# Kernel optimization log

Hardware: AMD Instinct MI355X
Metric: run time of the kernel (lower is better)

The kernel has to match this reference:

```python
import jax, jax.numpy as jnp
import numpy as np
import math

B, T, C, H = 2, 2048, 1024, 16
D = C // H

def setup_inputs() -> dict:
    key = jax.random.key(0)
    ks = jax.random.split(key, 10)
    s = 1.0 / math.sqrt(C)
    return {
        "x": jax.random.normal(ks[0], (B, T, C), jnp.float32),
        "x_query": jax.random.normal(ks[1], (B, T, C), jnp.float32),
        "Wq": jax.random.normal(ks[2], (C, C), jnp.float32) * s,
        "bq": jax.random.normal(ks[3], (C,), jnp.float32) * 0.02,
        "Wk": jax.random.normal(ks[4], (C, C), jnp.float32) * s,
        "bk": jax.random.normal(ks[5], (C,), jnp.float32) * 0.02,
        "Wv": jax.random.normal(ks[6], (C, C), jnp.float32) * s,
        "bv": jax.random.normal(ks[7], (C,), jnp.float32) * 0.02,
        "Wp": jax.random.normal(ks[8], (C, C), jnp.float32) * s,
        "bp": jax.random.normal(ks[9], (C,), jnp.float32) * 0.02,
    }

def reference(x, x_query, Wq, bq, Wk, bk, Wv, bv, Wp, bp):
    # torch nn.Linear: y = x @ W^T + b
    Tq = x_query.shape[1]
    Tk = x.shape[1]
    q = (x_query @ Wq.T + bq).reshape(B, Tq, H, D).transpose(0, 2, 1, 3)  # [B,H,Tq,D]
    k = (x @ Wk.T + bk).reshape(B, Tk, H, D).transpose(0, 2, 1, 3)       # [B,H,Tk,D]
    v = (x @ Wv.T + bv).reshape(B, Tk, H, D).transpose(0, 2, 1, 3)       # [B,H,Tk,D]
    scale = 1.0 / math.sqrt(D)
    att = jnp.einsum('bhqd,bhkd->bhqk', q, k) * scale                    # [B,H,Tq,Tk]
    # use_mask=True, past_kv=None -> causal tril mask over (Tq, Tk)
    mask = jnp.tril(jnp.ones((Tq, Tk), dtype=bool))
    att = jnp.where(mask[None, None, :, :], att, -jnp.inf)
    att = jax.nn.softmax(att, axis=-1)
    y = jnp.einsum('bhqk,bhkd->bhqd', att, v)                            # [B,H,Tq,D]
    y = y.transpose(0, 2, 1, 3).reshape(B, Tq, C)
    y = y @ Wp.T + bp
    return y
```

## Files before the change

kernel.cpp:

```cpp
#include <hip/hip_runtime.h>

typedef __bf16 bf16;
typedef __attribute__((ext_vector_type(8))) __bf16 bf16x8;
typedef __attribute__((ext_vector_type(4))) float f32x4;
typedef __attribute__((ext_vector_type(16))) float f32x16;
typedef __attribute__((ext_vector_type(4))) unsigned u32x4;

#define MFMA16(a, b, c) __builtin_amdgcn_mfma_f32_16x16x32_bf16((a), (b), (c), 0, 0, 0)
#define MFMA32(a, b, c) __builtin_amdgcn_mfma_f32_32x32x16_bf16((a), (b), (c), 0, 0, 0)
#define NEG_BIG (-1e30f)
#define SCL_LOG2 0.18033688011112042f
#define THR_RAW 44.3614195558365f

__device__ __forceinline__ void gload_lds16(void* lds, const void* g) {
  __builtin_amdgcn_global_load_lds(
      (const __attribute__((address_space(1))) void*)g,
      (__attribute__((address_space(3))) void*)lds, 16, 0, 0);
}

__device__ __forceinline__ unsigned pk2(float x, float y) {
  const unsigned short a = __builtin_bit_cast(unsigned short, (bf16)x);
  const unsigned short b = __builtin_bit_cast(unsigned short, (bf16)y);
  return (unsigned)a | ((unsigned)b << 16);
}

static __device__ const signed char KQT[32] =
  {15,15,10,10, 15,14,14,14,13, 9, 9, 4, 13,13,12,12, 8, 8,
   12,11,11,11, 7, 7, 3,  6, 6,  5, 5, 2,  1,  0};
static __device__ const signed char KSEG[32] =
  { 0, 1, 0, 1,  2, 0, 1, 2, 0, 0, 1, 0,  1, 2, 0, 1, 0, 1,
    2, 0, 1, 2, 0, 1, 0,  0, 1,  0, 1, 0,  0,  0};

__global__ void cvt6(const float* __restrict__ s0, const float* __restrict__ s1,
                     const float* __restrict__ s2, const float* __restrict__ s3,
                     const float* __restrict__ s4, const float* __restrict__ s5,
                     bf16* __restrict__ d0, bf16* __restrict__ d1,
                     bf16* __restrict__ d2, bf16* __restrict__ d3,
                     bf16* __restrict__ d4, bf16* __restrict__ d5) {
  const int c = blockIdx.x * blockDim.x + threadIdx.x;
  if (c >= 1572864) return;
  const float* s; bf16* d; int off;
  if (c < 524288)        { s = s0; d = d0; off = c; }
  else if (c < 1048576)  { s = s1; d = d1; off = c - 524288; }
  else {
    const int c2 = c - 1048576, seg = c2 >> 17;
    off = c2 & 131071;
    s = seg == 0 ? s2 : seg == 1 ? s3 : seg == 2 ? s4 : s5;
    d = seg == 0 ? d2 : seg == 1 ? d3 : seg == 2 ? d4 : d5;
  }
  const float4 a = ((const float4*)s)[off * 2 + 0];
  const float4 b = ((const float4*)s)[off * 2 + 1];
  bf16x8 o;
  o[0] = (bf16)a.x; o[1] = (bf16)a.y; o[2] = (bf16)a.z; o[3] = (bf16)a.w;
  o[4] = (bf16)b.x; o[5] = (bf16)b.y; o[6] = (bf16)b.z; o[7] = (bf16)b.w;
  ((bf16x8*)d)[off] = o;
}

__global__ void gemm_qkv(const bf16* __restrict__ XQ, const bf16* __restrict__ X,
                         const bf16* __restrict__ Wq, const bf16* __restrict__ Wk,
                         const bf16* __restrict__ Wv,
                         const float* __restrict__ bq, const float* __restrict__ bk,
                         const float* __restrict__ bv,
                         bf16* __restrict__ Qo, bf16* __restrict__ Ko,
                         bf16* __restrict__ Vto) {
  __shared__ __align__(16) bf16 As[128 * 32];
  __shared__ __align__(16) bf16 Bs[128 * 32];
  const int tid = threadIdx.x;
  const int wv = tid >> 6, lane = tid & 63;
  const int wr = wv >> 1, wc = wv & 1;
  const int lr = lane & 15, lg = lane >> 4;
  const int seg = blockIdx.x >> 3;
  const int n0 = (blockIdx.x & 7) * 128;
  const int m0 = blockIdx.y * 128;
  const bf16* __restrict__ A = seg == 0 ? XQ : X;
  const bf16* __restrict__ W = seg == 0 ? Wq : seg == 1 ? Wk : Wv;
  const float* __restrict__ bias = seg == 0 ? bq : seg == 1 ? bk : bv;
  const int K = 1024;

  f32x4 acc[4][4] = {};

  for (int k0 = 0; k0 < K; k0 += 32) {
    __syncthreads();
#pragma unroll
    for (int j = 0; j < 2; ++j) {
      const int e8 = (j * 256 + tid) * 8;
      const int row = e8 >> 5, col = e8 & 31;
      gload_lds16(As + (size_t)(j * 256 + wv * 64) * 8,
                  A + (size_t)(m0 + row) * K + k0 + col);
      gload_lds16(Bs + (size_t)(j * 256 + wv * 64) * 8,
                  W + (size_t)(n0 + row) * K + k0 + col);
    }
    __syncthreads();
    bf16x8 af[4], bfr[4];
#pragma unroll
    for (int i = 0; i < 4; ++i)
      af[i] = *(const bf16x8*)&As[(wr * 64 + i * 16 + lr) * 32 + lg * 8];
#pragma unroll
    for (int j = 0; j < 4; ++j)
      bfr[j] = *(const bf16x8*)&Bs[(wc * 64 + j * 16 + lr) * 32 + lg * 8];
#pragma unroll
    for (int i = 0; i < 4; ++i)
#pragma unroll
      for (int j = 0; j < 4; ++j)
        acc[i][j] = MFMA16(af[i], bfr[j], acc[i][j]);
  }

#pragma unroll
  for (int j = 0; j < 4; ++j) {
    const int n = n0 + wc * 64 + j * 16 + lr;
    const float bvv = bias[n];
    const int h = n >> 6, d = n & 63;
#pragma unroll
    for (int i = 0; i < 4; ++i) {
#pragma unroll
      for (int r = 0; r < 4; ++r) {
        const int m = m0 + wr * 64 + i * 16 + lg * 4 + r;
        const float v = acc[i][j][r] + bvv;
        const int b = m >> 11, t = m & 2047;
        if (seg == 0)      Qo[((size_t)(b * 16 + h) * 2048 + t) * 64 + d] = (bf16)v;
        else if (seg == 1) Ko[((size_t)(b * 16 + h) * 2048 + t) * 64 + d] = (bf16)v;
        else               Vto[((size_t)(b * 16 + h) * 64 + d) * 2048 + t] = (bf16)v;
      }
    }
  }
}

template <int BN>
__global__ void gemm_out(const bf16* __restrict__ A, const bf16* __restrict__ W,
                         const float* __restrict__ bias, float* __restrict__ out,
                         int M, int N, int K) {
  __shared__ __align__(16) bf16 As[128 * 32];
  __shared__ __align__(16) bf16 Bs[BN * 32];
  constexpr int NF = BN / 32;
  const int tid = threadIdx.x;
  const int wv = tid >> 6, lane = tid & 63;
  const int wr = wv >> 1, wc = wv & 1;
  const int lr = lane & 15, lg = lane >> 4;
  const int m0 = blockIdx.y * 128, n0 = blockIdx.x * BN;

  f32x4 acc[4][NF] = {};

  for (int k0 = 0; k0 < K; k0 += 32) {
    __syncthreads();
#pragma unroll
    for (int j = 0; j < 2; ++j) {
      const int e8 = (j * 256 + tid) * 8;
      const int row = e8 >> 5, col = e8 & 31;
      gload_lds16(As + (size_t)(j * 256 + wv * 64) * 8,
                  A + (size_t)(m0 + row) * K + k0 + col);
    }
#pragma unroll
    for (int j = 0; j < BN / 64; ++j) {
      const int e8 = (j * 256 + tid) * 8;
      const int row = e8 >> 5, col = e8 & 31;
      gload_lds16(Bs + (size_t)(j * 256 + wv * 64) * 8,
                  W + (size_t)(n0 + row) * K + k0 + col);
    }
    __syncthreads();
    bf16x8 af[4], bfr[NF];
#pragma unroll
    for (int i = 0; i < 4; ++i)
      af[i] = *(const bf16x8*)&As[(wr * 64 + i * 16 + lr) * 32 + lg * 8];
#pragma unroll
    for (int j = 0; j < NF; ++j)
      bfr[j] = *(const bf16x8*)&Bs[(wc * (BN / 2) + j * 16 + lr) * 32 + lg * 8];
#pragma unroll
    for (int i = 0; i < 4; ++i)
#pragma unroll
      for (int j = 0; j < NF; ++j)
        acc[i][j] = MFMA16(af[i], bfr[j], acc[i][j]);
  }

#pragma unroll
  for (int j = 0; j < NF; ++j) {
    const int n = n0 + wc * (BN / 2) + j * 16 + lr;
    const float bv = bias[n];
#pragma unroll
    for (int i = 0; i < 4; ++i) {
#pragma unroll
      for (int r = 0; r < 4; ++r) {
        const int m = m0 + wr * 64 + i * 16 + lg * 4 + r;
        out[(size_t)m * N + n] = acc[i][j][r] + bv;
      }
    }
  }
}

__global__ void attn_fwd(const bf16* __restrict__ Q, const bf16* __restrict__ Kk,
                         const bf16* __restrict__ Vt, bf16* __restrict__ attout,
                         bf16* __restrict__ Opart, float* __restrict__ Ml) {
  __shared__ __align__(16) char Ks[2][8192];
  __shared__ __align__(16) char Vs[2][8192];

  const int tid = threadIdx.x;
  const int wv = tid >> 6, lane = tid & 63;
  const int q31 = lane & 31, hi = lane >> 5, l7 = lane & 7;
  const int kind = blockIdx.x >> 5, bh = blockIdx.x & 31;
  const int qt = KQT[kind], seg = KSEG[kind];
  const int nt = 2 * qt + 2;
  const int ns = qt >= 11 ? 3 : (qt >= 5 ? 2 : 1);
  const int t0 = (nt * seg) / ns, t1 = (nt * (seg + 1)) / ns;
  const bool split = ns > 1;

  const int q0 = qt * 128;
  const int qs = q0 + wv * 32;
  const int qa = qs + q31;
  const size_t bhT = (size_t)bh * 2048;
  const bf16* Vh = Vt + (size_t)bh * 64 * 2048;

  bf16x8 qf[4];
#pragma unroll
  for (int kw = 0; kw < 4; ++kw)
    qf[kw] = *(const bf16x8*)(Q + (bhT + qa) * 64 + kw * 16 + hi * 8);

  u32x4 onesu; onesu[0] = onesu[1] = onesu[2] = onesu[3] = 0x3F803F80u;
  const bf16x8 ones8 = __builtin_bit_cast(bf16x8, onesu);

  f32x16 O0 = {}, O1 = {};
  f32x16 Ol = {};
  float m2 = NEG_BIG;

  auto STAGE = [&](int buf, int kv0) {
#pragma unroll
    for (int rr = 0; rr < 2; ++rr) {
      const int c = rr * 256 + tid;
      const int row = c >> 3, cc = c & 7;
      const int gcol = (cc ^ (row & 7)) * 8;
      gload_lds16(Ks[buf] + (rr * 256 + wv * 64) * 16,
                  Kk + (bhT + kv0 + row) * 64 + gcol);
      gload_lds16(Vs[buf] + (rr * 256 + wv * 64) * 16,
                  Vh + (size_t)row * 2048 + kv0 + gcol);
    }
  };

  STAGE(0, t0 * 64);
  __syncthreads();

  for (int it = t0; it < t1; ++it) {
    const int kv0 = it * 64;
    const int cur = (it - t0) & 1;
    if (it + 1 < t1) STAGE(cur ^ 1, (it + 1) * 64);

    if (kv0 <= qs + 31) {
      f32x16 S0 = {}, S1 = {};
      __builtin_amdgcn_s_setprio(1);
#pragma unroll
      for (int kw = 0; kw < 4; ++kw) {
        const int cb = (32 * kw + 16 * hi) ^ (l7 << 4);
        const bf16x8 k0 = *(const bf16x8*)(Ks[cur] + q31 * 128 + cb);
        const bf16x8 k1 = *(const bf16x8*)(Ks[cur] + (32 + q31) * 128 + cb);
        S0 = MFMA32(k0, qf[kw], S0);
        S1 = MFMA32(k1, qf[kw], S1);
      }
      __builtin_amdgcn_s_setprio(0);

      float p[32];
#pragma unroll
      for (int r = 0; r < 16; ++r) { p[r] = S0[r]; p[16 + r] = S1[r]; }
      if (kv0 + 63 > qs) {
#pragma unroll
        for (int a = 0; a < 2; ++a)
#pragma unroll
          for (int r = 0; r < 16; ++r) {
            const int kva = kv0 + a * 32 + (r & 3) + 8 * (r >> 2) + 4 * hi;
            if (kva > qa) p[a * 16 + r] = NEG_BIG;
          }
      }

      float w16[16];
#pragma unroll
      for (int i = 0; i < 16; ++i) w16[i] = fmaxf(p[i], p[i + 16]);
#pragma unroll
      for (int i = 0; i < 8; ++i) w16[i] = fmaxf(w16[i], w16[i + 8]);
#pragma unroll
      for (int i = 0; i < 4; ++i) w16[i] = fmaxf(w16[i], w16[i + 4]);
      float mx = fmaxf(fmaxf(w16[0], w16[1]), fmaxf(w16[2], w16[3]));
      mx = fmaxf(mx, __shfl_xor(mx, 32));
      if (!__all(mx - m2 <= THR_RAW)) {
        const float mnew = fmaxf(m2, mx);
        const float fac = exp2f((m2 - mnew) * SCL_LOG2);
#pragma unroll
        for (int r = 0; r < 16; ++r) { O0[r] *= fac; O1[r] *= fac; }
        Ol[0] *= fac;
        m2 = mnew;
      }
      const float nm2 = -m2 * SCL_LOG2;
#pragma unroll
      for (int i = 0; i < 32; ++i) p[i] = exp2f(__builtin_fmaf(p[i], SCL_LOG2, nm2));

      bf16x8 pf[4];
#pragma unroll
      for (int ks = 0; ks < 4; ++ks) {
        const int base = 16 * (ks >> 1) + 8 * (ks & 1);
        const unsigned g0 = pk2(p[base + 0], p[base + 1]);
        const unsigned g1 = pk2(p[base + 2], p[base + 3]);
        const unsigned g2 = pk2(p[base + 4], p[base + 5]);
        const unsigned g3 = pk2(p[base + 6], p[base + 7]);
        const unsigned e0 = __shfl_xor(hi ? g0 : g2, 32);
        const unsigned e1 = __shfl_xor(hi ? g1 : g3, 32);
        u32x4 w4;
        w4[0] = hi ? e0 : g0;
        w4[1] = hi ? e1 : g1;
        w4[2] = hi ? g2 : e0;
        w4[3] = hi ? g3 : e1;
        pf[ks] = __builtin_bit_cast(bf16x8, w4);
      }

      __builtin_amdgcn_s_setprio(1);
#pragma unroll
      for (int ks = 0; ks < 4; ++ks) {
        const int cb = (32 * ks + 16 * hi) ^ (l7 << 4);
        const bf16x8 v0 = *(const bf16x8*)(Vs[cur] + q31 * 128 + cb);
        const bf16x8 v1 = *(const bf16x8*)(Vs[cur] + (32 + q31) * 128 + cb);
        O0 = MFMA32(v0, pf[ks], O0);
        O1 = MFMA32(v1, pf[ks], O1);
        Ol = MFMA32(ones8, pf[ks], Ol);
      }
      __builtin_amdgcn_s_setprio(0);
    }
    __syncthreads();
  }

  const float l = Ol[0];
  if (!split) {
    const int b = bh >> 4, h = bh & 15;
    const float inv = 1.f / l;
    bf16* orow = attout + ((size_t)b * 2048 + qa) * 1024 + h * 64;
#pragma unroll
    for (int r = 0; r < 16; ++r) {
      const int dd = (r & 3) + 8 * (r >> 2) + 4 * hi;
      orow[dd]      = (bf16)(O0[r] * inv);
      orow[32 + dd] = (bf16)(O1[r] * inv);
    }
  } else {
    const int sbase = (qt < 11) ? (qt - 5) * 2 : 12 + (qt - 11) * 3;
    const int slot = bh * 27 + sbase + seg;
    bf16* Po = Opart + (size_t)slot * 8192;
    const int row = wv * 32 + q31;
#pragma unroll
    for (int r = 0; r < 16; ++r) {
      const int dd = (r & 3) + 8 * (r >> 2) + 4 * hi;
      Po[row * 64 + dd]      = (bf16)O0[r];
      Po[row * 64 + 32 + dd] = (bf16)O1[r];
    }
    Ml[slot * 256 + row]       = m2;
    Ml[slot * 256 + 128 + row] = l;
  }
}

__global__ void attn_combine(const bf16* __restrict__ Opart,
                             const float* __restrict__ Ml,
                             bf16* __restrict__ attout) {
  const int u = blockIdx.x;
  const int bh = u / 11, qti = u - bh * 11;
  const int qt = qti + 5;
  const int ns = qt >= 11 ? 3 : 2;
  const int sbase = (qt < 11) ? (qt - 5) * 2 : 12 + (qt - 11) * 3;
  const int s0 = bh * 27 + sbase;
  const int tid = threadIdx.x;
  const int row = tid >> 1, c0 = (tid & 1) * 32;

  float m[3], lv[3];
  float M = NEG_BIG;
#pragma unroll
  for (int s = 0; s < 3; ++s)
    if (s < ns) {
      m[s] = Ml[(s0 + s) * 256 + row];
      lv[s] = Ml[(s0 + s) * 256 + 128 + row];
      M = fmaxf(M, m[s]);
    }
  float w[3], L = 0.f;
#pragma unroll
  for (int s = 0; s < 3; ++s)
    if (s < ns) {
      w[s] = exp2f((m[s] - M) * SCL_LOG2);
      L += w[s] * lv[s];
    }
  const float inv = 1.f / L;

  float acc[32] = {};
#pragma unroll
  for (int s = 0; s < 3; ++s)
    if (s < ns) {
      const bf16* p = Opart + (size_t)(s0 + s) * 8192 + row * 64 + c0;
      const float ws = w[s];
#pragma unroll
      for (int j = 0; j < 4; ++j) {
        const bf16x8 v = *(const bf16x8*)(p + j * 8);
#pragma unroll
        for (int e = 0; e < 8; ++e) acc[j * 8 + e] += ws * (float)v[e];
      }
    }

  const int b = bh >> 4, h = bh & 15, t = qt * 128 + row;
  bf16* dst = attout + ((size_t)b * 2048 + t) * 1024 + h * 64 + c0;
#pragma unroll
  for (int d = 0; d < 32; ++d) dst[d] = (bf16)(acc[d] * inv);
}

extern "C" void kernel_launch(void* const* d_in, const int* in_sizes, int n_in,
                              void* d_out, int out_size, void* d_ws, size_t ws_size,
                              hipStream_t stream) {
  const float* x   = (const float*)d_in[0];
  const float* xq  = (const float*)d_in[1];
  const float* Wq  = (const float*)d_in[2];
  const float* bq  = (const float*)d_in[3];
  const float* Wk  = (const float*)d_in[4];
  const float* bk  = (const float*)d_in[5];
  const float* Wv  = (const float*)d_in[6];
  const float* bv  = (const float*)d_in[7];
  const float* Wp  = (const float*)d_in[8];
  const float* bp  = (const float*)d_in[9];
  float* out = (float*)d_out;

  const size_t NTC = 4194304;
  const size_t NW  = 1048576;
  bf16* ws = (bf16*)d_ws;
  bf16* XQb = ws;
  bf16* Xb  = XQb + NTC;
  bf16* Wqb = Xb + NTC;
  bf16* Wkb = Wqb + NW;
  bf16* Wvb = Wkb + NW;
  bf16* Wpb = Wvb + NW;
  bf16* Qw  = Wpb + NW;
  bf16* Kw  = Qw + NTC;
  bf16* Vtw = Kw + NTC;
  bf16* Aw  = Vtw + NTC;
  bf16* Opart = (bf16*)d_ws;
  float* Ml   = (float*)(Aw + NTC);

  dim3 blk(256);
  cvt6<<<dim3(6144), blk, 0, stream>>>(xq, x, Wq, Wk, Wv, Wp,
                                       XQb, Xb, Wqb, Wkb, Wvb, Wpb);
  gemm_qkv<<<dim3(24, 32), blk, 0, stream>>>(XQb, Xb, Wqb, Wkb, Wvb,
                                             bq, bk, bv, Qw, Kw, Vtw);
  attn_fwd<<<dim3(1024), blk, 0, stream>>>(Qw, Kw, Vtw, Aw, Opart, Ml);
  attn_combine<<<dim3(352), blk, 0, stream>>>(Opart, Ml, Aw);
  gemm_out<64><<<dim3(16, 32), blk, 0, stream>>>(Aw, Wpb, bp, out, 4096, 1024, 1024);
}
```

Before: 128.2 us.

## Double GEMM K-tile to 64 with XOR-swizzled LDS layout

Both projection GEMMs now stage a 64-wide K slice per iteration instead of 32, halving the number of barrier pairs and global-load issue rounds. The LDS rows are 128 bytes, so the 16-byte chunks are XOR-swizzled by row to avoid bank conflicts on the MFMA fragment reads. Each staged tile is consumed in two MFMA halves. Shared memory per block grows (32KB for qkv), which may lower occupancy, and the gemm_out template parameter is removed in favor of a fixed BN of 64.

```diff
diff --git a/kernel.cpp b/kernel.cpp
--- a/kernel.cpp
+++ b/kernel.cpp
@@ -63,8 +63,8 @@
                          const float* __restrict__ bv,
                          bf16* __restrict__ Qo, bf16* __restrict__ Ko,
                          bf16* __restrict__ Vto) {
-  __shared__ __align__(16) bf16 As[128 * 32];
-  __shared__ __align__(16) bf16 Bs[128 * 32];
+  __shared__ __align__(16) char As[128 * 128];
+  __shared__ __align__(16) char Bs[128 * 128];
   const int tid = threadIdx.x;
   const int wv = tid >> 6, lane = tid & 63;
   const int wr = wv >> 1, wc = wv & 1;
@@ -79,30 +79,39 @@
 
   f32x4 acc[4][4] = {};
 
-  for (int k0 = 0; k0 < K; k0 += 32) {
+  for (int k0 = 0; k0 < K; k0 += 64) {
     __syncthreads();
 #pragma unroll
-    for (int j = 0; j < 2; ++j) {
-      const int e8 = (j * 256 + tid) * 8;
-      const int row = e8 >> 5, col = e8 & 31;
-      gload_lds16(As + (size_t)(j * 256 + wv * 64) * 8,
-                  A + (size_t)(m0 + row) * K + k0 + col);
-      gload_lds16(Bs + (size_t)(j * 256 + wv * 64) * 8,
-                  W + (size_t)(n0 + row) * K + k0 + col);
+    for (int j = 0; j < 4; ++j) {
+      const int c = j * 256 + tid;
+      const int row = c >> 3, cc = c & 7;
+      const int gcol = (cc ^ (row & 7)) * 8;
+      gload_lds16(As + (j * 256 + wv * 64) * 16,
+                  A + (size_t)(m0 + row) * K + k0 + gcol);
+      gload_lds16(Bs + (j * 256 + wv * 64) * 16,
+                  W + (size_t)(n0 + row) * K + k0 + gcol);
     }
     __syncthreads();
-    bf16x8 af[4], bfr[4];
-#pragma unroll
-    for (int i = 0; i < 4; ++i)
-      af[i] = *(const bf16x8*)&As[(wr * 64 + i * 16 + lr) * 32 + lg * 8];
-#pragma unroll
-    for (int j = 0; j < 4; ++j)
-      bfr[j] = *(const bf16x8*)&Bs[(wc * 64 + j * 16 + lr) * 32 + lg * 8];
-#pragma unroll
-    for (int i = 0; i < 4; ++i)
-#pragma unroll
-      for (int j = 0; j < 4; ++j)
-        acc[i][j] = MFMA16(af[i], bfr[j], acc[i][j]);
+#pragma unroll
+    for (int half = 0; half < 2; ++half) {
+      const int kb = half * 64 + lg * 16;
+      bf16x8 af[4], bfr[4];
+#pragma unroll
+      for (int i = 0; i < 4; ++i) {
+        const int row = wr * 64 + i * 16 + lr;
+        af[i] = *(const bf16x8*)(As + row * 128 + (kb ^ ((row & 7) << 4)));
+      }
+#pragma unroll
+      for (int j = 0; j < 4; ++j) {
+        const int row = wc * 64 + j * 16 + lr;
+        bfr[j] = *(const bf16x8*)(Bs + row * 128 + (kb ^ ((row & 7) << 4)));
+      }
+#pragma unroll
+      for (int i = 0; i < 4; ++i)
+#pragma unroll
+        for (int j = 0; j < 4; ++j)
+          acc[i][j] = MFMA16(af[i], bfr[j], acc[i][j]);
+    }
   }
 
 #pragma unroll
@@ -125,55 +134,63 @@
   }
 }
 
-template <int BN>
 __global__ void gemm_out(const bf16* __restrict__ A, const bf16* __restrict__ W,
                          const float* __restrict__ bias, float* __restrict__ out,
                          int M, int N, int K) {
-  __shared__ __align__(16) bf16 As[128 * 32];
-  __shared__ __align__(16) bf16 Bs[BN * 32];
-  constexpr int NF = BN / 32;
+  __shared__ __align__(16) char As[128 * 128];
+  __shared__ __align__(16) char Bs[64 * 128];
   const int tid = threadIdx.x;
   const int wv = tid >> 6, lane = tid & 63;
   const int wr = wv >> 1, wc = wv & 1;
   const int lr = lane & 15, lg = lane >> 4;
-  const int m0 = blockIdx.y * 128, n0 = blockIdx.x * BN;
-
-  f32x4 acc[4][NF] = {};
-
-  for (int k0 = 0; k0 < K; k0 += 32) {
+  const int m0 = blockIdx.y * 128, n0 = blockIdx.x * 64;
+
+  f32x4 acc[4][2] = {};
+
+  for (int k0 = 0; k0 < K; k0 += 64) {
     __syncthreads();
 #pragma unroll
+    for (int j = 0; j < 4; ++j) {
+      const int c = j * 256 + tid;
+      const int row = c >> 3, cc = c & 7;
+      const int gcol = (cc ^ (row & 7)) * 8;
+      gload_lds16(As + (j * 256 + wv * 64) * 16,
+                  A + (size_t)(m0 + row) * K + k0 + gcol);
+    }
+#pragma unroll
     for (int j = 0; j < 2; ++j) {
-      const int e8 = (j * 256 + tid) * 8;
-      const int row = e8 >> 5, col = e8 & 31;
-      gload_lds16(As + (size_t)(j * 256 + wv * 64) * 8,
-                  A + (size_t)(m0 + row) * K + k0 + col);
-    }
-#pragma unroll
-    for (int j = 0; j < BN / 64; ++j) {
-      const int e8 = (j * 256 + tid) * 8;
-      const int row = e8 >> 5, col = e8 & 31;
-      gload_lds16(Bs + (size_t)(j * 256 + wv * 64) * 8,
-                  W + (size_t)(n0 + row) * K + k0 + col);
+      const int c = j * 256 + tid;
+      const int row = c >> 3, cc = c & 7;
+      const int gcol = (cc ^ (row & 7)) * 8;
+      gload_lds16(Bs + (j * 256 + wv * 64) * 16,
+                  W + (size_t)(n0 + row) * K + k0 + gcol);
     }
     __syncthreads();
-    bf16x8 af[4], bfr[NF];
-#pragma unroll
-    for (int i = 0; i < 4; ++i)
-      af[i] = *(const bf16x8*)&As[(wr * 64 + i * 16 + lr) * 32 + lg * 8];
-#pragma unroll
-    for (int j = 0; j < NF; ++j)
-      bfr[j] = *(const bf16x8*)&Bs[(wc * (BN / 2) + j * 16 + lr) * 32 + lg * 8];
-#pragma unroll
-    for (int i = 0; i < 4; ++i)
-#pragma unroll
-      for (int j = 0; j < NF; ++j)
-        acc[i][j] = MFMA16(af[i], bfr[j], acc[i][j]);
-  }
-
-#pragma unroll
-  for (int j = 0; j < NF; ++j) {
-    const int n = n0 + wc * (BN / 2) + j * 16 + lr;
+#pragma unroll
+    for (int half = 0; half < 2; ++half) {
+      const int kb = half * 64 + lg * 16;
+      bf16x8 af[4], bfr[2];
+#pragma unroll
+      for (int i = 0; i < 4; ++i) {
+        const int row = wr * 64 + i * 16 + lr;
+        af[i] = *(const bf16x8*)(As + row * 128 + (kb ^ ((row & 7) << 4)));
+      }
+#pragma unroll
+      for (int j = 0; j < 2; ++j) {
+        const int row = wc * 32 + j * 16 + lr;
+        bfr[j] = *(const bf16x8*)(Bs + row * 128 + (kb ^ ((row & 7) << 4)));
+      }
+#pragma unroll
+      for (int i = 0; i < 4; ++i)
+#pragma unroll
+        for (int j = 0; j < 2; ++j)
+          acc[i][j] = MFMA16(af[i], bfr[j], acc[i][j]);
+    }
+  }
+
+#pragma unroll
+  for (int j = 0; j < 2; ++j) {
+    const int n = n0 + wc * 32 + j * 16 + lr;
     const float bv = bias[n];
 #pragma unroll
     for (int i = 0; i < 4; ++i) {
@@ -436,5 +453,5 @@
                                              bq, bk, bv, Qw, Kw, Vtw);
   attn_fwd<<<dim3(1024), blk, 0, stream>>>(Qw, Kw, Vtw, Aw, Opart, Ml);
   attn_combine<<<dim3(352), blk, 0, stream>>>(Opart, Ml, Aw);
-  gemm_out<64><<<dim3(16, 32), blk, 0, stream>>>(Aw, Wpb, bp, out, 4096, 1024, 1024);
-}
+  gemm_out<<<dim3(16, 32), blk, 0, stream>>>(Aw, Wpb, bp, out, 4096, 1024, 1024);
+}
```

After: 118.6 us, median of 3. -7.5%, faster.
